# Kernel tuning notes

Measured on AMD Instinct MI355X. Metric: run time of the kernel, lower is better.

The kernel has to match this reference:

```python
import jax, jax.numpy as jnp
import numpy as np

DIM = 4096
N_HEADS = 32
N_KV_HEADS = 8
HEAD_DIM = DIM // N_HEADS  # 128
B, S = 2, 2048
LN_EPS = 1e-5


def _precompute_freqs_cis(seqlen, head_dim, theta=10000.0):
    inv = 1.0 / (theta ** (np.arange(0, head_dim, 2, dtype=np.float32) / head_dim))  # [HD/2]
    ang = np.outer(np.arange(seqlen, dtype=np.float32), inv)  # [S, HD/2]
    return jnp.asarray(np.stack([np.cos(ang), np.sin(ang)], axis=-1))  # [S, HD/2, 2]


def setup_inputs() -> dict:
    key = jax.random.key(0)
    ks = jax.random.split(key, 9)
    std = 0.02
    return {
        "x": jax.random.normal(ks[0], (B, S, DIM), dtype=jnp.float32),
        "freqs_cis": _precompute_freqs_cis(S, HEAD_DIM),
        "wq": jax.random.normal(ks[1], (N_HEADS * HEAD_DIM, DIM), dtype=jnp.float32) * std,
        "wk": jax.random.normal(ks[2], (N_KV_HEADS * HEAD_DIM, DIM), dtype=jnp.float32) * std,
        "wv": jax.random.normal(ks[3], (N_KV_HEADS * HEAD_DIM, DIM), dtype=jnp.float32) * std,
        "wo": jax.random.normal(ks[4], (DIM, N_HEADS * HEAD_DIM), dtype=jnp.float32) * std,
        "q_norm_w": jnp.ones((N_HEADS * HEAD_DIM,), dtype=jnp.float32),
        "q_norm_b": jnp.zeros((N_HEADS * HEAD_DIM,), dtype=jnp.float32),
        "k_norm_w": jnp.ones((N_KV_HEADS * HEAD_DIM,), dtype=jnp.float32),
        "k_norm_b": jnp.zeros((N_KV_HEADS * HEAD_DIM,), dtype=jnp.float32),
    }


def _layernorm(v, w, b):
    mu = jnp.mean(v, axis=-1, keepdims=True)
    var = jnp.var(v, axis=-1, keepdims=True)
    return (v - mu) * jax.lax.rsqrt(var + LN_EPS) * w + b


def _rope(t, fc):
    # t: [B, S, nh, HD]; fc: [S, HD/2, 2] = (cos, sin)
    b_, s_, nh, hd = t.shape
    tr = t.reshape(b_, s_, nh, hd // 2, 2)
    a, bb = tr[..., 0], tr[..., 1]
    cos = fc[None, :, None, :, 0]
    sin = fc[None, :, None, :, 1]
    out = jnp.stack([a * cos - bb * sin, a * sin + bb * cos], axis=-1)
    return out.reshape(t.shape)


def reference(x, freqs_cis, wq, wk, wv, wo, q_norm_w, q_norm_b, k_norm_w, k_norm_b):
    bsz, seqlen, _ = x.shape
    H, KV, HD = N_HEADS, N_KV_HEADS, HEAD_DIM
    R = H // KV  # GQA repeat factor

    xq = jnp.einsum('bsd,ed->bse', x, wq)
    xk = jnp.einsum('bsd,ed->bse', x, wk)
    xv = jnp.einsum('bsd,ed->bse', x, wv)

    xq = _layernorm(xq, q_norm_w, q_norm_b)
    xk = _layernorm(xk, k_norm_w, k_norm_b)

    xq = xq.reshape(bsz, seqlen, H, HD)
    xk = xk.reshape(bsz, seqlen, KV, HD)
    xv = xv.reshape(bsz, seqlen, KV, HD)

    xq = _rope(xq, freqs_cis)
    xk = _rope(xk, freqs_cis)

    # GQA: group q heads as (kv, rep) and broadcast k/v instead of materializing repeats
    xqg = xq.reshape(bsz, seqlen, KV, R, HD)
    scale = 1.0 / jnp.sqrt(jnp.float32(HD))
    scores = jnp.einsum('bqkrh,bskh->bkrqs', xqg, xk) * scale  # [B,KV,R,S,S]
    attn = jax.nn.softmax(scores, axis=-1)
    out = jnp.einsum('bkrqs,bskh->bqkrh', attn, xv).reshape(bsz, seqlen, H * HD)
    return jnp.einsum('bse,de->bsd', out, wo)
```

## Files before the change

kernel.cpp:

```cpp
#include <hip/hip_runtime.h>
#include <cstdint>

typedef _Float16 half4v __attribute__((ext_vector_type(4)));
typedef _Float16 half8v __attribute__((ext_vector_type(8)));
typedef __fp16   fp16x2 __attribute__((ext_vector_type(2)));
typedef float    f32x4v __attribute__((ext_vector_type(4)));

#define DIM    4096
#define SEQ    2048
#define NBATCH 2
#define NHEAD  32
#define NKVH   8
#define HDIM   128
#define MROWS  (NBATCH*SEQ)
#define QKV_N  6144
#define KOFF   4096
#define VOFF   5120

__device__ __forceinline__ void gl_lds16(const void* g, void* l) {
  __builtin_amdgcn_global_load_lds(
      (const __attribute__((address_space(1))) void*)g,
      (__attribute__((address_space(3))) void*)l, 16, 0, 0);
}

__global__ __launch_bounds__(256) void cvt_kernel(const float* __restrict__ in,
                                                  _Float16* __restrict__ out, int n8) {
  int stride = gridDim.x * blockDim.x;
  for (int i = blockIdx.x * blockDim.x + threadIdx.x; i < n8; i += stride) {
    const float4* p = (const float4*)(in + (size_t)i * 8);
    float4 a = p[0], b = p[1];
    half8v h;
    h[0] = (_Float16)a.x; h[1] = (_Float16)a.y; h[2] = (_Float16)a.z; h[3] = (_Float16)a.w;
    h[4] = (_Float16)b.x; h[5] = (_Float16)b.y; h[6] = (_Float16)b.z; h[7] = (_Float16)b.w;
    *(half8v*)(out + (size_t)i * 8) = h;
  }
}


#define SBAR() do { asm volatile("" ::: "memory"); \
                    __builtin_amdgcn_s_barrier();  \
                    asm volatile("" ::: "memory"); } while (0)
#define LGK0() asm volatile("s_waitcnt lgkmcnt(0)" ::: "memory")
#define VM6()  asm volatile("s_waitcnt vmcnt(6)" ::: "memory")
#define VM4()  asm volatile("s_waitcnt vmcnt(4)" ::: "memory")
#define VM0()  asm volatile("s_waitcnt vmcnt(0)" ::: "memory")

#define STAGE_HALF(Gm, rowbase, kidx, h, buf) do {                                   \
    gl_lds16((Gm) + (size_t)((rowbase) + (h)*128 + srow) * K + (kidx)*64 + sslot8,   \
             (buf) + (h)*8192 + w*512);                                              \
    gl_lds16((Gm) + (size_t)((rowbase) + (h)*128 + 64 + srow) * K + (kidx)*64 + sslot8, \
             (buf) + (h)*8192 + 4096 + w*512);                                       \
  } while (0)

#define MFMA_Q(hm, hn, bf)                                                   \
    _Pragma("unroll") for (int kk = 0; kk < 2; ++kk)                         \
      _Pragma("unroll") for (int mi = 0; mi < 4; ++mi)                       \
        _Pragma("unroll") for (int ni = 0; ni < 2; ++ni)                     \
          acc[(hm) * 4 + mi][(hn) * 2 + ni] =                                \
              __builtin_amdgcn_mfma_f32_16x16x32_f16(                        \
                  a[mi][kk], bf[ni][kk], acc[(hm) * 4 + mi][(hn) * 2 + ni], 0, 0, 0)

#define KSTEP(kcur, AC, BC, AN)                                              \
  do {                                                                       \
    const int k_ = (kcur);                                                   \
    half8v a[4][2], b0[2][2], b1[2][2];                                      \
                                         \
    _Pragma("unroll") for (int mi = 0; mi < 4; ++mi)                         \
      _Pragma("unroll") for (int kk = 0; kk < 2; ++kk)                       \
        a[mi][kk] = *(const half8v*)((AC) + (wm * 128 + mi * 16 + li) * 64 + \
                                     (((kk * 4 + g) ^ li7) * 8));            \
    _Pragma("unroll") for (int ni = 0; ni < 2; ++ni)                         \
      _Pragma("unroll") for (int kk = 0; kk < 2; ++kk)                       \
        b0[ni][kk] = *(const half8v*)((BC) + (wn * 64 + ni * 16 + li) * 64 + \
                                      (((kk * 4 + g) ^ li7) * 8));           \
    if (k_ + 1 < nkt) STAGE_HALF(A, bm, k_ + 1, 1, (AN));                    \
    SBAR(); LGK0();                                                          \
    __builtin_amdgcn_s_setprio(1);                                           \
    MFMA_Q(0, 0, b0);                                                        \
    __builtin_amdgcn_s_setprio(0);                                           \
    SBAR();                                                                  \
                                         \
    _Pragma("unroll") for (int ni = 0; ni < 2; ++ni)                         \
      _Pragma("unroll") for (int kk = 0; kk < 2; ++kk)                       \
        b1[ni][kk] = *(const half8v*)((BC) + (wn * 64 + 32 + ni * 16 + li) * 64 + \
                                      (((kk * 4 + g) ^ li7) * 8));           \
    SBAR(); LGK0();                                                          \
    __builtin_amdgcn_s_setprio(1);                                           \
    MFMA_Q(0, 1, b1);                                                        \
    __builtin_amdgcn_s_setprio(0);                                           \
    SBAR();                                                                  \
          \
    _Pragma("unroll") for (int mi = 0; mi < 4; ++mi)                         \
      _Pragma("unroll") for (int kk = 0; kk < 2; ++kk)                       \
        a[mi][kk] = *(const half8v*)((AC) + (wm * 128 + 64 + mi * 16 + li) * 64 + \
                                     (((kk * 4 + g) ^ li7) * 8));            \
    if (k_ + 2 < nkt) {                                                      \
      STAGE_HALF(B, bn, k_ + 2, 0, (BC));                                    \
      STAGE_HALF(B, bn, k_ + 2, 1, (BC));                                    \
    }                                                                        \
    SBAR(); LGK0();                                                          \
    __builtin_amdgcn_s_setprio(1);                                           \
    MFMA_Q(1, 1, b1);                                                        \
    __builtin_amdgcn_s_setprio(0);                                           \
    SBAR();                                                                  \
          \
    if (k_ + 2 < nkt) STAGE_HALF(A, bm, k_ + 2, 0, (AC));                    \
    SBAR();                                                                  \
    __builtin_amdgcn_s_setprio(1);                                           \
    MFMA_Q(1, 0, b0);                                                        \
    __builtin_amdgcn_s_setprio(0);                                           \
    if (k_ + 2 < nkt) { VM6(); } else if (k_ + 1 < nkt) { VM0(); }           \
    SBAR();                                                                  \
  } while (0)

template<int OUTF16>
__global__ __launch_bounds__(512, 2) void gemm256(const _Float16* __restrict__ A,
                                                  const _Float16* __restrict__ B,
                                                  void* __restrict__ Cp,
                                                  int N, int K, int nbx) {
  __shared__ __align__(16) _Float16 As[2][256 * 64];
  __shared__ __align__(16) _Float16 Bs[2][256 * 64];
  const int tid = threadIdx.x, lane = tid & 63, w = tid >> 6;
  const int g = lane >> 4, li = lane & 15, li7 = lane & 7;
  const int wm = w >> 2, wn = w & 3;
  const int nwg = gridDim.x, orig = blockIdx.x;
  const int wgid = (nwg & 7) ? orig : ((orig & 7) * (nwg >> 3) + (orig >> 3));
  const int bm = (wgid / nbx) * 256, bn = (wgid % nbx) * 256;
  const int srow = tid >> 3;
  const int sslot8 = ((lane & 7) ^ ((lane >> 3) & 7)) * 8;
  const int nkt = K >> 6;
  _Float16* As0 = &As[0][0]; _Float16* As1 = &As[1][0];
  _Float16* Bs0 = &Bs[0][0]; _Float16* Bs1 = &Bs[1][0];

  f32x4v acc[8][4] = {};

  STAGE_HALF(A, bm, 0, 0, As0);
  STAGE_HALF(A, bm, 0, 1, As0);
  STAGE_HALF(B, bn, 0, 0, Bs0);
  STAGE_HALF(B, bn, 0, 1, Bs0);
  if (nkt > 1) {
    STAGE_HALF(B, bn, 1, 0, Bs1);
    STAGE_HALF(B, bn, 1, 1, Bs1);
    STAGE_HALF(A, bm, 1, 0, As1);
    VM6();
  } else {
    VM0();
  }
  SBAR();

  for (int k = 0; k < nkt; k += 2) {
    KSTEP(k,     As0, Bs0, As1);
    KSTEP(k + 1, As1, Bs1, As0);
  }

  const int r0 = bm + wm * 128 + g * 4;
  const int c0 = bn + wn * 64 + li;
#pragma unroll
  for (int mi = 0; mi < 8; ++mi)
#pragma unroll
    for (int ni = 0; ni < 4; ++ni)
#pragma unroll
      for (int j = 0; j < 4; ++j) {
        size_t idx = (size_t)(r0 + mi * 16 + j) * N + (c0 + ni * 16);
        if (OUTF16) ((_Float16*)Cp)[idx] = (_Float16)acc[mi][ni][j];
        else        ((float*)Cp)[idx]    = acc[mi][ni][j];
      }
}

template<int E>
__global__ __launch_bounds__(256) void ln_rope(_Float16* __restrict__ t, int ldt,
                                               const float* __restrict__ gw,
                                               const float* __restrict__ gb,
                                               const float* __restrict__ fc) {
  constexpr int EPT = E / 256;
  const int row = blockIdx.x;
  const int s = row & (SEQ - 1);
  const int tid = threadIdx.x, lane = tid & 63, w = tid >> 6;
  _Float16* rp = t + (size_t)row * ldt + tid * EPT;
  float v[EPT];
#pragma unroll
  for (int i = 0; i < EPT; i += 4) {
    half4v hv = *(const half4v*)(rp + i);
    v[i] = (float)hv[0]; v[i+1] = (float)hv[1]; v[i+2] = (float)hv[2]; v[i+3] = (float)hv[3];
  }
  float sum = 0.f, ssq = 0.f;
#pragma unroll
  for (int i = 0; i < EPT; ++i) { sum += v[i]; ssq += v[i] * v[i]; }
#pragma unroll
  for (int off = 1; off < 64; off <<= 1) { sum += __shfl_xor(sum, off); ssq += __shfl_xor(ssq, off); }
  __shared__ float red[8];
  if (lane == 0) { red[w] = sum; red[4 + w] = ssq; }
  __syncthreads();
  sum = red[0] + red[1] + red[2] + red[3];
  ssq = red[4] + red[5] + red[6] + red[7];
  const float mu = sum * (1.0f / E);
  const float rstd = rsqrtf(ssq * (1.0f / E) - mu * mu + 1e-5f);
  float ov[EPT];
#pragma unroll
  for (int i = 0; i < EPT; i += 2) {
    int e = tid * EPT + i;
    int hd = e & (HDIM - 1);
    float2 cs = *(const float2*)(fc + (size_t)s * HDIM + (hd >> 1) * 2);
    float a = (v[i]   - mu) * rstd * gw[e]   + gb[e];
    float b = (v[i+1] - mu) * rstd * gw[e+1] + gb[e+1];
    ov[i]   = a * cs.x - b * cs.y;
    ov[i+1] = a * cs.y + b * cs.x;
  }
#pragma unroll
  for (int i = 0; i < EPT; i += 4) {
    half4v hv;
    hv[0] = (_Float16)ov[i];   hv[1] = (_Float16)ov[i+1];
    hv[2] = (_Float16)ov[i+2]; hv[3] = (_Float16)ov[i+3];
    *(half4v*)(rp + i) = hv;
  }
}

__global__ __launch_bounds__(256) void vtrans(const _Float16* __restrict__ qkv,
                                              _Float16* __restrict__ vt) {
  __shared__ _Float16 tile[64][136];
  const int blk = blockIdx.x;
  const int st = blk & 31, kvh = (blk >> 5) & 7, b = blk >> 8;
  const int t = threadIdx.x;
  const _Float16* src = qkv + (size_t)(b * SEQ + st * 64) * QKV_N + VOFF + kvh * 128;
#pragma unroll
  for (int i = 0; i < 4; ++i) {
    int sl = (t >> 4) + i * 16;
    int h0 = (t & 15) * 8;
    *(half8v*)&tile[sl][h0] = *(const half8v*)(src + (size_t)sl * QKV_N + h0);
  }
  __syncthreads();
  const int hd = t & 127, half = t >> 7;
  _Float16* dst = vt + ((size_t)((b * NKVH + kvh) * 128 + hd)) * SEQ + st * 64 + half * 32;
#pragma unroll
  for (int j = 0; j < 32; j += 8) {
    half8v v;
#pragma unroll
    for (int e = 0; e < 8; ++e) v[e] = tile[half * 32 + j + e][hd];
    *(half8v*)(dst + j) = v;
  }
}

__global__ __launch_bounds__(256, 2) void attn_kernel(const _Float16* __restrict__ QKV,
                                                      const _Float16* __restrict__ VT,
                                                      _Float16* __restrict__ Oa) {
  __shared__ __align__(16) _Float16 Ksh[2][64 * 128];
  __shared__ __align__(16) char Vsh[128 * 128];
  const int tid = threadIdx.x, lane = tid & 63, w = tid >> 6;
  const int g = lane >> 4, li = lane & 15;
  const int blk = blockIdx.x;
  const int qt = blk & 31, h = (blk >> 5) & 31, b = blk >> 10;
  const int kvh = h >> 2;
  const size_t LD = QKV_N;
  const _Float16* Qb = QKV + (size_t)(b * SEQ) * LD + h * HDIM;
  const _Float16* Kb = QKV + (size_t)(b * SEQ) * LD + KOFF + kvh * HDIM;
  const _Float16* VTb = VT + (size_t)((b * NKVH + kvh) * 128) * SEQ;
  const int lg = lane >> 4;
  const int gbit = (lane >> 5) & 1;

  const int qrow = qt * 64 + w * 16 + li;
  half8v qf[4];
#pragma unroll
  for (int kk = 0; kk < 4; ++kk) {
    half8v q0 = *(const half8v*)(Qb + (size_t)qrow * LD + kk * 32 + g * 8);
#pragma unroll
    for (int e = 0; e < 8; ++e) q0[e] = q0[e] * (_Float16)0.08838834764831845f;
    qf[kk] = q0;
  }
  float mrow = -1e30f, lrow = 0.f;
  f32x4v oacc[8] = {};

#define ASTAGE_K(kt_, buf_) do {                                              \
    _Pragma("unroll") for (int i_ = 0; i_ < 4; ++i_) {                        \
      int chunk = i_ * 4 + w;                                                 \
      int r = chunk * 4 + lg;                                                 \
      int sc8 = ((lane & 15) ^ (r & 7)) * 8;                                  \
      gl_lds16(Kb + (size_t)((kt_) * 64 + r) * LD + sc8, (buf_) + chunk * 512); \
    } } while (0)

#define ASTAGE_V(kt_, buf_) do {                                              \
    _Pragma("unroll") for (int i_ = 0; i_ < 4; ++i_) {                        \
      int chunk = i_ * 4 + w;                                                 \
      int hd_ = chunk * 8 + (lane >> 3);                                      \
      int keyh = (chunk ^ (lane >> 3)) & 7;                                   \
      int p_ = lane & 7;                                                      \
      gl_lds16(VTb + (size_t)hd_ * SEQ + (kt_) * 64 + ((p_ ^ keyh) * 8),      \
               (buf_) + chunk * 1024);                                        \
    } } while (0)

  ASTAGE_K(0, Ksh[0]);
  ASTAGE_V(0, Vsh);
  VM0();
  SBAR();

  const int NT = SEQ / 64;
  for (int kt = 0; kt < NT; ++kt) {
    const int cur = kt & 1;
    const _Float16* Kcur = Ksh[cur];
    f32x4v sc[4] = {};
    __builtin_amdgcn_s_setprio(1);
#pragma unroll
    for (int kk = 0; kk < 4; ++kk) {
#pragma unroll
      for (int ni = 0; ni < 4; ++ni) {
        half8v kf = *(const half8v*)(Kcur + (16 * ni + li) * 128 + ((4 * kk + g) ^ (li & 7)) * 8);
        sc[ni] = __builtin_amdgcn_mfma_f32_16x16x32_f16(kf, qf[kk], sc[ni], 0, 0, 0);
      }
    }
    __builtin_amdgcn_s_setprio(0);
    if (kt + 1 < NT) ASTAGE_K(kt + 1, Ksh[cur ^ 1]);
    float m16 = sc[0][0];
#pragma unroll
    for (int ni = 0; ni < 4; ++ni) {
      m16 = fmaxf(m16, fmaxf(fmaxf(sc[ni][0], sc[ni][1]), fmaxf(sc[ni][2], sc[ni][3])));
    }
    m16 = fmaxf(m16, __shfl_xor(m16, 16));
    m16 = fmaxf(m16, __shfl_xor(m16, 32));
    if (!__all(m16 - mrow <= 8.0f)) {
      const float mn = fmaxf(mrow, m16);
      const float sfo = __expf(mrow - mn);
      mrow = mn;
      lrow *= sfo;
      float sfj[4];
#pragma unroll
      for (int j = 0; j < 4; ++j) sfj[j] = __shfl(sfo, (lane & 48) | (4 * g + j));
#pragma unroll
      for (int nio = 0; nio < 8; ++nio) {
        oacc[nio][0] *= sfj[0]; oacc[nio][1] *= sfj[1];
        oacc[nio][2] *= sfj[2]; oacc[nio][3] *= sfj[3];
      }
    }
    float pp[4][4];
    float rs = 0.f;
#pragma unroll
    for (int ni = 0; ni < 4; ++ni)
#pragma unroll
      for (int j = 0; j < 4; ++j) { float pv = __expf(sc[ni][j] - mrow); pp[ni][j] = pv; rs += pv; }
    rs += __shfl_xor(rs, 16); rs += __shfl_xor(rs, 32);
    lrow += rs;
    uint32_t u[4][2];
#pragma unroll
    for (int ni = 0; ni < 4; ++ni) {
      fp16x2 p0 = __builtin_amdgcn_cvt_pkrtz(pp[ni][0], pp[ni][1]);
      fp16x2 p1 = __builtin_amdgcn_cvt_pkrtz(pp[ni][2], pp[ni][3]);
      u[ni][0] = *(uint32_t*)&p0;
      u[ni][1] = *(uint32_t*)&p1;
    }
    if (kt + 1 < NT) { VM4(); } else { VM0(); }
    SBAR();
#pragma unroll
    for (int kk = 0; kk < 2; ++kk) {
      uint32_t own0 = gbit ? u[2*kk+1][0] : u[2*kk][0];
      uint32_t own1 = gbit ? u[2*kk+1][1] : u[2*kk][1];
      uint32_t oth0 = gbit ? u[2*kk][0]   : u[2*kk+1][0];
      uint32_t oth1 = gbit ? u[2*kk][1]   : u[2*kk+1][1];
      uint32_t r16_0 = (uint32_t)__shfl_xor((int)own0, 16);
      uint32_t r16_1 = (uint32_t)__shfl_xor((int)own1, 16);
      uint32_t r32_0 = (uint32_t)__shfl_xor((int)oth0, 32);
      uint32_t r32_1 = (uint32_t)__shfl_xor((int)oth1, 32);
      uint32_t r48_0 = (uint32_t)__shfl_xor((int)oth0, 48);
      uint32_t r48_1 = (uint32_t)__shfl_xor((int)oth1, 48);
      uint32_t d0 = (g == 0) ? own0 : (g == 1) ? r48_0 : (g == 2) ? r32_0 : r16_0;
      uint32_t d1 = (g == 0) ? own1 : (g == 1) ? r48_1 : (g == 2) ? r32_1 : r16_1;
      uint32_t d2 = (g == 0) ? r16_0 : (g == 1) ? r32_0 : (g == 2) ? r48_0 : own0;
      uint32_t d3 = (g == 0) ? r16_1 : (g == 1) ? r32_1 : (g == 2) ? r48_1 : own1;
      union { uint32_t u4[4]; half8v hh; } pa;
      pa.u4[0] = d0; pa.u4[1] = d1; pa.u4[2] = d2; pa.u4[3] = d3;
      __builtin_amdgcn_s_setprio(1);
#pragma unroll
      for (int nio = 0; nio < 8; ++nio) {
        int r = nio * 16 + li;
        int key = ((r >> 3) ^ r) & 7;
        half8v bv = *(const half8v*)(Vsh + r * 128 + (((kk * 4 + g) ^ key) << 4));
        oacc[nio] = __builtin_amdgcn_mfma_f32_16x16x32_f16(pa.hh, bv, oacc[nio], 0, 0, 0);
      }
      __builtin_amdgcn_s_setprio(0);
    }
    VM0();
    SBAR();
    if (kt + 1 < NT) ASTAGE_V(kt + 1, Vsh);
  }
#undef ASTAGE_K
#undef ASTAGE_V
  float rinv[4];
#pragma unroll
  for (int j = 0; j < 4; ++j)
    rinv[j] = 1.0f / __shfl(lrow, (lane & 48) | (4 * g + j));
  _Float16* Ob = Oa + (size_t)(b * SEQ + qt * 64 + w * 16) * DIM + h * HDIM;
#pragma unroll
  for (int j = 0; j < 4; ++j)
#pragma unroll
    for (int nio = 0; nio < 8; ++nio)
      Ob[(size_t)(4 * g + j) * DIM + nio * 16 + li] = (_Float16)(oacc[nio][j] * rinv[j]);
}

extern "C" void kernel_launch(void* const* d_in, const int* in_sizes, int n_in,
                              void* d_out, int out_size, void* d_ws, size_t ws_size,
                              hipStream_t stream) {
  const float* x   = (const float*)d_in[0];
  const float* fc  = (const float*)d_in[1];
  const float* wq  = (const float*)d_in[2];
  const float* wk  = (const float*)d_in[3];
  const float* wv  = (const float*)d_in[4];
  const float* wo  = (const float*)d_in[5];
  const float* qnw = (const float*)d_in[6];
  const float* qnb = (const float*)d_in[7];
  const float* knw = (const float*)d_in[8];
  const float* knb = (const float*)d_in[9];
  float* out = (float*)d_out;
  (void)in_sizes; (void)n_in; (void)out_size;

  const size_t MB = 1024 * 1024;
  if (ws_size < 128 * MB) return;
  char* ws = (char*)d_ws;
  _Float16* x_h    = (_Float16*)(ws + 0);
  _Float16* wqkv_h = (_Float16*)(ws + 32 * MB);
  _Float16* wk_h   = (_Float16*)(ws + 64 * MB);
  _Float16* wv_h   = (_Float16*)(ws + 72 * MB);
  _Float16* qkv_h  = (_Float16*)(ws + 80 * MB);
  _Float16* wo_h   = wqkv_h;
  _Float16* vt_h   = wk_h;
  _Float16* ao_h   = x_h;

  cvt_kernel<<<2048, 256, 0, stream>>>(x,  x_h,    (MROWS * DIM) / 8);
  cvt_kernel<<<2048, 256, 0, stream>>>(wq, wqkv_h, (DIM * DIM) / 8);
  cvt_kernel<<<1024, 256, 0, stream>>>(wk, wk_h,   (1024 * DIM) / 8);
  cvt_kernel<<<1024, 256, 0, stream>>>(wv, wv_h,   (1024 * DIM) / 8);

  gemm256<1><<<(MROWS / 256) * (QKV_N / 256), 512, 0, stream>>>(x_h, wqkv_h, qkv_h,
                                                                QKV_N, DIM, QKV_N / 256);

  cvt_kernel<<<2048, 256, 0, stream>>>(wo, wo_h, (DIM * DIM) / 8);

  vtrans<<<NBATCH * NKVH * (SEQ / 64), 256, 0, stream>>>(qkv_h, vt_h);

  ln_rope<4096><<<MROWS, 256, 0, stream>>>(qkv_h,        QKV_N, qnw, qnb, fc);
  ln_rope<1024><<<MROWS, 256, 0, stream>>>(qkv_h + KOFF, QKV_N, knw, knb, fc);

  attn_kernel<<<NBATCH * NHEAD * (SEQ / 64), 256, 0, stream>>>(qkv_h, vt_h, ao_h);

  gemm256<0><<<(MROWS / 256) * (DIM / 256), 512, 0, stream>>>(ao_h, wo_h, out,
                                                              DIM, DIM, DIM / 256);
}
```

Baseline: 688.5 us.

## Double attention query tile per block to 128 rows, two 16-row subtiles per wave

Each attention block now handles 128 query rows instead of 64, with each wave processing two 16-row query subtiles that share every K and V fragment loaded from LDS. This halves the K/V global-to-LDS staging traffic and LDS reads per query, and halves the grid size. It costs roughly double the accumulator and score registers, which may reduce occupancy under launch_bounds(256,2), and the smaller grid (1024 blocks) may underfill the GPU.

```diff
diff --git a/kernel.cpp b/kernel.cpp
--- a/kernel.cpp
+++ b/kernel.cpp
@@ -35,7 +35,6 @@
     *(half8v*)(out + (size_t)i * 8) = h;
   }
 }
-
 
 #define SBAR() do { asm volatile("" ::: "memory"); \
                     __builtin_amdgcn_s_barrier();  \
@@ -248,7 +247,7 @@
   const int tid = threadIdx.x, lane = tid & 63, w = tid >> 6;
   const int g = lane >> 4, li = lane & 15;
   const int blk = blockIdx.x;
-  const int qt = blk & 31, h = (blk >> 5) & 31, b = blk >> 10;
+  const int qt = blk & 15, h = (blk >> 4) & 31, b = blk >> 9;
   const int kvh = h >> 2;
   const size_t LD = QKV_N;
   const _Float16* Qb = QKV + (size_t)(b * SEQ) * LD + h * HDIM;
@@ -257,17 +256,20 @@
   const int lg = lane >> 4;
   const int gbit = (lane >> 5) & 1;
 
-  const int qrow = qt * 64 + w * 16 + li;
-  half8v qf[4];
-#pragma unroll
-  for (int kk = 0; kk < 4; ++kk) {
-    half8v q0 = *(const half8v*)(Qb + (size_t)qrow * LD + kk * 32 + g * 8);
-#pragma unroll
-    for (int e = 0; e < 8; ++e) q0[e] = q0[e] * (_Float16)0.08838834764831845f;
-    qf[kk] = q0;
-  }
-  float mrow = -1e30f, lrow = 0.f;
-  f32x4v oacc[8] = {};
+  half8v qf[2][4];
+#pragma unroll
+  for (int s = 0; s < 2; ++s) {
+    const int qrow = qt * 128 + w * 32 + s * 16 + li;
+#pragma unroll
+    for (int kk = 0; kk < 4; ++kk) {
+      half8v q0 = *(const half8v*)(Qb + (size_t)qrow * LD + kk * 32 + g * 8);
+#pragma unroll
+      for (int e = 0; e < 8; ++e) q0[e] = q0[e] * (_Float16)0.08838834764831845f;
+      qf[s][kk] = q0;
+    }
+  }
+  float mrow[2] = {-1e30f, -1e30f}, lrow[2] = {0.f, 0.f};
+  f32x4v oacc[2][8] = {};
 
 #define ASTAGE_K(kt_, buf_) do {                                              \
     _Pragma("unroll") for (int i_ = 0; i_ < 4; ++i_) {                        \
@@ -296,82 +298,91 @@
   for (int kt = 0; kt < NT; ++kt) {
     const int cur = kt & 1;
     const _Float16* Kcur = Ksh[cur];
-    f32x4v sc[4] = {};
+    f32x4v sc0[4] = {}, sc1[4] = {};
     __builtin_amdgcn_s_setprio(1);
 #pragma unroll
     for (int kk = 0; kk < 4; ++kk) {
 #pragma unroll
       for (int ni = 0; ni < 4; ++ni) {
         half8v kf = *(const half8v*)(Kcur + (16 * ni + li) * 128 + ((4 * kk + g) ^ (li & 7)) * 8);
-        sc[ni] = __builtin_amdgcn_mfma_f32_16x16x32_f16(kf, qf[kk], sc[ni], 0, 0, 0);
+        sc0[ni] = __builtin_amdgcn_mfma_f32_16x16x32_f16(kf, qf[0][kk], sc0[ni], 0, 0, 0);
+        sc1[ni] = __builtin_amdgcn_mfma_f32_16x16x32_f16(kf, qf[1][kk], sc1[ni], 0, 0, 0);
       }
     }
     __builtin_amdgcn_s_setprio(0);
     if (kt + 1 < NT) ASTAGE_K(kt + 1, Ksh[cur ^ 1]);
-    float m16 = sc[0][0];
-#pragma unroll
-    for (int ni = 0; ni < 4; ++ni) {
-      m16 = fmaxf(m16, fmaxf(fmaxf(sc[ni][0], sc[ni][1]), fmaxf(sc[ni][2], sc[ni][3])));
-    }
-    m16 = fmaxf(m16, __shfl_xor(m16, 16));
-    m16 = fmaxf(m16, __shfl_xor(m16, 32));
-    if (!__all(m16 - mrow <= 8.0f)) {
-      const float mn = fmaxf(mrow, m16);
-      const float sfo = __expf(mrow - mn);
-      mrow = mn;
-      lrow *= sfo;
-      float sfj[4];
-#pragma unroll
-      for (int j = 0; j < 4; ++j) sfj[j] = __shfl(sfo, (lane & 48) | (4 * g + j));
-#pragma unroll
-      for (int nio = 0; nio < 8; ++nio) {
-        oacc[nio][0] *= sfj[0]; oacc[nio][1] *= sfj[1];
-        oacc[nio][2] *= sfj[2]; oacc[nio][3] *= sfj[3];
-      }
-    }
-    float pp[4][4];
-    float rs = 0.f;
-#pragma unroll
-    for (int ni = 0; ni < 4; ++ni)
-#pragma unroll
-      for (int j = 0; j < 4; ++j) { float pv = __expf(sc[ni][j] - mrow); pp[ni][j] = pv; rs += pv; }
-    rs += __shfl_xor(rs, 16); rs += __shfl_xor(rs, 32);
-    lrow += rs;
-    uint32_t u[4][2];
-#pragma unroll
-    for (int ni = 0; ni < 4; ++ni) {
-      fp16x2 p0 = __builtin_amdgcn_cvt_pkrtz(pp[ni][0], pp[ni][1]);
-      fp16x2 p1 = __builtin_amdgcn_cvt_pkrtz(pp[ni][2], pp[ni][3]);
-      u[ni][0] = *(uint32_t*)&p0;
-      u[ni][1] = *(uint32_t*)&p1;
+    uint32_t u[2][4][2];
+#pragma unroll
+    for (int s = 0; s < 2; ++s) {
+      f32x4v* sc = s ? sc1 : sc0;
+      float m16 = sc[0][0];
+#pragma unroll
+      for (int ni = 0; ni < 4; ++ni)
+        m16 = fmaxf(m16, fmaxf(fmaxf(sc[ni][0], sc[ni][1]), fmaxf(sc[ni][2], sc[ni][3])));
+      m16 = fmaxf(m16, __shfl_xor(m16, 16));
+      m16 = fmaxf(m16, __shfl_xor(m16, 32));
+      if (!__all(m16 - mrow[s] <= 8.0f)) {
+        const float mn = fmaxf(mrow[s], m16);
+        const float sfo = __expf(mrow[s] - mn);
+        mrow[s] = mn;
+        lrow[s] *= sfo;
+        float sfj[4];
+#pragma unroll
+        for (int j = 0; j < 4; ++j) sfj[j] = __shfl(sfo, (lane & 48) | (4 * g + j));
+#pragma unroll
+        for (int nio = 0; nio < 8; ++nio) {
+          oacc[s][nio][0] *= sfj[0]; oacc[s][nio][1] *= sfj[1];
+          oacc[s][nio][2] *= sfj[2]; oacc[s][nio][3] *= sfj[3];
+        }
+      }
+      float rs = 0.f;
+#pragma unroll
+      for (int ni = 0; ni < 4; ++ni)
+#pragma unroll
+        for (int j = 0; j < 4; ++j) { float pv = __expf(sc[ni][j] - mrow[s]); sc[ni][j] = pv; rs += pv; }
+      rs += __shfl_xor(rs, 16); rs += __shfl_xor(rs, 32);
+      lrow[s] += rs;
+#pragma unroll
+      for (int ni = 0; ni < 4; ++ni) {
+        fp16x2 p0 = __builtin_amdgcn_cvt_pkrtz(sc[ni][0], sc[ni][1]);
+        fp16x2 p1 = __builtin_amdgcn_cvt_pkrtz(sc[ni][2], sc[ni][3]);
+        u[s][ni][0] = *(uint32_t*)&p0;
+        u[s][ni][1] = *(uint32_t*)&p1;
+      }
     }
     if (kt + 1 < NT) { VM4(); } else { VM0(); }
     SBAR();
 #pragma unroll
     for (int kk = 0; kk < 2; ++kk) {
-      uint32_t own0 = gbit ? u[2*kk+1][0] : u[2*kk][0];
-      uint32_t own1 = gbit ? u[2*kk+1][1] : u[2*kk][1];
-      uint32_t oth0 = gbit ? u[2*kk][0]   : u[2*kk+1][0];
-      uint32_t oth1 = gbit ? u[2*kk][1]   : u[2*kk+1][1];
-      uint32_t r16_0 = (uint32_t)__shfl_xor((int)own0, 16);
-      uint32_t r16_1 = (uint32_t)__shfl_xor((int)own1, 16);
-      uint32_t r32_0 = (uint32_t)__shfl_xor((int)oth0, 32);
-      uint32_t r32_1 = (uint32_t)__shfl_xor((int)oth1, 32);
-      uint32_t r48_0 = (uint32_t)__shfl_xor((int)oth0, 48);
-      uint32_t r48_1 = (uint32_t)__shfl_xor((int)oth1, 48);
-      uint32_t d0 = (g == 0) ? own0 : (g == 1) ? r48_0 : (g == 2) ? r32_0 : r16_0;
-      uint32_t d1 = (g == 0) ? own1 : (g == 1) ? r48_1 : (g == 2) ? r32_1 : r16_1;
-      uint32_t d2 = (g == 0) ? r16_0 : (g == 1) ? r32_0 : (g == 2) ? r48_0 : own0;
-      uint32_t d3 = (g == 0) ? r16_1 : (g == 1) ? r32_1 : (g == 2) ? r48_1 : own1;
-      union { uint32_t u4[4]; half8v hh; } pa;
-      pa.u4[0] = d0; pa.u4[1] = d1; pa.u4[2] = d2; pa.u4[3] = d3;
+      half8v pa[2];
+#pragma unroll
+      for (int s = 0; s < 2; ++s) {
+        uint32_t own0 = gbit ? u[s][2*kk+1][0] : u[s][2*kk][0];
+        uint32_t own1 = gbit ? u[s][2*kk+1][1] : u[s][2*kk][1];
+        uint32_t oth0 = gbit ? u[s][2*kk][0]   : u[s][2*kk+1][0];
+        uint32_t oth1 = gbit ? u[s][2*kk][1]   : u[s][2*kk+1][1];
+        uint32_t r16_0 = (uint32_t)__shfl_xor((int)own0, 16);
+        uint32_t r16_1 = (uint32_t)__shfl_xor((int)own1, 16);
+        uint32_t r32_0 = (uint32_t)__shfl_xor((int)oth0, 32);
+        uint32_t r32_1 = (uint32_t)__shfl_xor((int)oth1, 32);
+        uint32_t r48_0 = (uint32_t)__shfl_xor((int)oth0, 48);
+        uint32_t r48_1 = (uint32_t)__shfl_xor((int)oth1, 48);
+        uint32_t d0 = (g == 0) ? own0 : (g == 1) ? r48_0 : (g == 2) ? r32_0 : r16_0;
+        uint32_t d1 = (g == 0) ? own1 : (g == 1) ? r48_1 : (g == 2) ? r32_1 : r16_1;
+        uint32_t d2 = (g == 0) ? r16_0 : (g == 1) ? r32_0 : (g == 2) ? r48_0 : own0;
+        uint32_t d3 = (g == 0) ? r16_1 : (g == 1) ? r32_1 : (g == 2) ? r48_1 : own1;
+        union { uint32_t u4[4]; half8v hh; } pu;
+        pu.u4[0] = d0; pu.u4[1] = d1; pu.u4[2] = d2; pu.u4[3] = d3;
+        pa[s] = pu.hh;
+      }
       __builtin_amdgcn_s_setprio(1);
 #pragma unroll
       for (int nio = 0; nio < 8; ++nio) {
         int r = nio * 16 + li;
         int key = ((r >> 3) ^ r) & 7;
         half8v bv = *(const half8v*)(Vsh + r * 128 + (((kk * 4 + g) ^ key) << 4));
-        oacc[nio] = __builtin_amdgcn_mfma_f32_16x16x32_f16(pa.hh, bv, oacc[nio], 0, 0, 0);
+        oacc[0][nio] = __builtin_amdgcn_mfma_f32_16x16x32_f16(pa[0], bv, oacc[0][nio], 0, 0, 0);
+        oacc[1][nio] = __builtin_amdgcn_mfma_f32_16x16x32_f16(pa[1], bv, oacc[1][nio], 0, 0, 0);
       }
       __builtin_amdgcn_s_setprio(0);
     }
@@ -381,16 +392,19 @@
   }
 #undef ASTAGE_K
 #undef ASTAGE_V
-  float rinv[4];
-#pragma unroll
-  for (int j = 0; j < 4; ++j)
-    rinv[j] = 1.0f / __shfl(lrow, (lane & 48) | (4 * g + j));
-  _Float16* Ob = Oa + (size_t)(b * SEQ + qt * 64 + w * 16) * DIM + h * HDIM;
-#pragma unroll
-  for (int j = 0; j < 4; ++j)
-#pragma unroll
-    for (int nio = 0; nio < 8; ++nio)
-      Ob[(size_t)(4 * g + j) * DIM + nio * 16 + li] = (_Float16)(oacc[nio][j] * rinv[j]);
+#pragma unroll
+  for (int s = 0; s < 2; ++s) {
+    float rinv[4];
+#pragma unroll
+    for (int j = 0; j < 4; ++j)
+      rinv[j] = 1.0f / __shfl(lrow[s], (lane & 48) | (4 * g + j));
+    _Float16* Ob = Oa + (size_t)(b * SEQ + qt * 128 + w * 32 + s * 16) * DIM + h * HDIM;
+#pragma unroll
+    for (int j = 0; j < 4; ++j)
+#pragma unroll
+      for (int nio = 0; nio < 8; ++nio)
+        Ob[(size_t)(4 * g + j) * DIM + nio * 16 + li] = (_Float16)(oacc[s][nio][j] * rinv[j]);
+  }
 }
 
 extern "C" void kernel_launch(void* const* d_in, const int* in_sizes, int n_in,
@@ -436,7 +450,7 @@
   ln_rope<4096><<<MROWS, 256, 0, stream>>>(qkv_h,        QKV_N, qnw, qnb, fc);
   ln_rope<1024><<<MROWS, 256, 0, stream>>>(qkv_h + KOFF, QKV_N, knw, knb, fc);
 
-  attn_kernel<<<NBATCH * NHEAD * (SEQ / 64), 256, 0, stream>>>(qkv_h, vt_h, ao_h);
+  attn_kernel<<<NBATCH * NHEAD * (SEQ / 128), 256, 0, stream>>>(qkv_h, vt_h, ao_h);
 
   gemm256<0><<<(MROWS / 256) * (DIM / 256), 512, 0, stream>>>(ao_h, wo_h, out,
                                                               DIM, DIM, DIM / 256);
```

New measurement: 649.8 us. 1.06x faster.
